# Kernel tuning notes

Measured on AMD Instinct MI355X. Metric: run time of the kernel, lower is better.

## Reference

```python
import jax, jax.numpy as jnp
import numpy as np

B, T, D, U = 32, 2048, 1024, 1024

def setup_inputs() -> dict:
    key = jax.random.key(0)
    ks = jax.random.split(key, 8)
    s = 0.02
    return {
        "query": jax.random.normal(ks[0], (B, D), dtype=jnp.float32),
        "values": jax.random.normal(ks[1], (B, T, D), dtype=jnp.float32),
        "W1": jax.random.normal(ks[2], (D, U), dtype=jnp.float32) * s,
        "b1": jnp.zeros((U,), dtype=jnp.float32),
        "W2": jax.random.normal(ks[3], (D, U), dtype=jnp.float32) * s,
        "b2": jnp.zeros((U,), dtype=jnp.float32),
        "V": jax.random.normal(ks[4], (U, 1), dtype=jnp.float32) * s,
        "bv": jnp.zeros((1,), dtype=jnp.float32),
    }

def reference(query, values, W1, b1, W2, b2, V, bv):
    # query: [B, D] -> [B, 1, U] via W2; values: [B, T, D] -> [B, T, U] via W1
    q_proj = query @ W2 + b2                     # [B, U]
    v_proj = jnp.einsum('btd,du->btu', values, W1) + b1   # [B, T, U]
    # score: Dense(1) on tanh(sum) -> [B, T, 1]
    score = jnp.tanh(v_proj + q_proj[:, None, :]) @ V + bv  # [B, T, 1]
    attention_weights = jax.nn.softmax(score, axis=1)        # softmax over time
    context_vector = jnp.sum(attention_weights * values, axis=1)  # [B, D]
    return context_vector, attention_weights
```

## Files before the change

kernel.cpp:

```cpp
#include <hip/hip_runtime.h>
#include <hip/hip_bf16.h>
#include <stdint.h>

#define WS_W1F   0
#define WS_QP2   2097152
#define WS_SCORE (2097152 + 131072)

typedef __attribute__((ext_vector_type(8))) short bf16x8;
typedef __attribute__((ext_vector_type(4))) float f32x4;

__device__ inline uint16_t f2b(float f) {
    __hip_bfloat16 h = __float2bfloat16(f);
    return *reinterpret_cast<uint16_t*>(&h);
}

__global__ __launch_bounds__(256) void k_prep(const float* __restrict__ W1,
                                              const float* __restrict__ query,
                                              const float* __restrict__ W2,
                                              const float* __restrict__ b1,
                                              const float* __restrict__ b2,
                                              __hip_bfloat16* __restrict__ W1f,
                                              float* __restrict__ qp2,
                                              float* __restrict__ ctx_out) {
    int blk = blockIdx.x, tid = threadIdx.x;
    if (blk < 256) {
        int lane = tid & 63, fi = tid >> 6;
        int l15 = lane & 15, quad = lane >> 4;
        #pragma unroll
        for (int p = 0; p < 2; ++p) {
            int frag = blk * 8 + p * 4 + fi;
            int ut = frag >> 5, ks = frag & 31;
            union { uint16_t h[8]; int4 v; } pk;
            #pragma unroll
            for (int j = 0; j < 8; ++j) {
                float x = W1[(size_t)(ks * 32 + quad * 8 + j) * 1024 + ut * 16 + l15];
                pk.h[j] = f2b(x);
            }
            *(int4*)((char*)W1f + (size_t)frag * 1024 + lane * 16) = pk.v;
        }
    } else {
        int b = blk - 256;
        int u = tid * 4;
        *(float4*)(ctx_out + b * 1024 + u) = make_float4(0.f, 0.f, 0.f, 0.f);
        float4 a;
        a.x = b1[u] + b2[u];     a.y = b1[u+1] + b2[u+1];
        a.z = b1[u+2] + b2[u+2]; a.w = b1[u+3] + b2[u+3];
        const float* q = query + b * 1024;
        #pragma unroll 8
        for (int d = 0; d < 1024; ++d) {
            float qd = q[d];
            float4 wv = *(const float4*)(W2 + (size_t)d * 1024 + u);
            a.x += qd * wv.x; a.y += qd * wv.y; a.z += qd * wv.z; a.w += qd * wv.w;
        }
        *(float4*)(qp2 + b * 1024 + u) = a;
    }
}

__global__ __launch_bounds__(512, 1) void k_score(
        const float* __restrict__ values, const __hip_bfloat16* __restrict__ W1f,
        const float* __restrict__ qp2, const float* __restrict__ V,
        float* __restrict__ score) {
    extern __shared__ char smem[];
    uint16_t* Al = (uint16_t*)smem;
    float* red = (float*)(smem + 131072);

    const int tid = threadIdx.x;
    const int lane = tid & 63, w = tid >> 6;
    const int quad = lane >> 4, l15 = lane & 15;
    const int b = blockIdx.x >> 5, trow0 = (blockIdx.x & 31) << 6;

    const float* Ag = values + (size_t)(b * 2048 + trow0) * 1024;
    #pragma unroll
    for (int i = 0; i < 16; ++i) {
        int id = i * 512 + tid;
        int row = id >> 7, c = id & 127;
        const float* src = Ag + (size_t)row * 1024 + c * 8;
        float4 v0 = *(const float4*)src;
        float4 v1 = *(const float4*)(src + 4);
        union { uint16_t h[8]; int4 v; } pk;
        pk.h[0]=f2b(v0.x); pk.h[1]=f2b(v0.y); pk.h[2]=f2b(v0.z); pk.h[3]=f2b(v0.w);
        pk.h[4]=f2b(v1.x); pk.h[5]=f2b(v1.y); pk.h[6]=f2b(v1.z); pk.h[7]=f2b(v1.w);
        int pos = (c & 112) | ((c & 15) ^ (row & 15));
        *(int4*)(Al + (size_t)row * 1024 + pos * 8) = pk.v;
    }
    __syncthreads();

    const char* Bbase = (const char*)W1f + (size_t)(w * 8) * 32768 + lane * 16;

    f32x4 acc[4][8];
    #pragma unroll
    for (int rt = 0; rt < 4; ++rt)
        #pragma unroll
        for (int ct = 0; ct < 8; ++ct) acc[rt][ct] = (f32x4){0.f, 0.f, 0.f, 0.f};

    bf16x8 af[2][4], bfr[2][8];
    {
        int pos = (quad & 15) ^ l15;
        #pragma unroll
        for (int rt = 0; rt < 4; ++rt)
            af[0][rt] = *(bf16x8*)(Al + (rt * 16 + l15) * 1024 + pos * 8);
        #pragma unroll
        for (int ct = 0; ct < 8; ++ct)
            bfr[0][ct] = *(const bf16x8*)(Bbase + (size_t)(ct * 32) * 1024);
    }

    #pragma unroll 2
    for (int ks = 0; ks < 32; ++ks) {
        int cur = ks & 1, nxt = cur ^ 1;
        if (ks < 31) {
            int cb = (ks + 1) * 4 + quad;
            int pos = (cb & 112) | ((cb & 15) ^ l15);
            #pragma unroll
            for (int rt = 0; rt < 4; ++rt)
                af[nxt][rt] = *(bf16x8*)(Al + (rt * 16 + l15) * 1024 + pos * 8);
            #pragma unroll
            for (int ct = 0; ct < 8; ++ct)
                bfr[nxt][ct] = *(const bf16x8*)(Bbase + (size_t)(ct * 32 + ks + 1) * 1024);
        }
        #pragma unroll
        for (int rt = 0; rt < 4; ++rt)
            #pragma unroll
            for (int ct = 0; ct < 8; ++ct)
                acc[rt][ct] = __builtin_amdgcn_mfma_f32_16x16x32_bf16(
                    af[cur][rt], bfr[cur][ct], acc[rt][ct], 0, 0, 0);
    }

    float srow[4][4];
    #pragma unroll
    for (int rt = 0; rt < 4; ++rt)
        #pragma unroll
        for (int r = 0; r < 4; ++r) srow[rt][r] = 0.f;
    #pragma unroll
    for (int ct = 0; ct < 8; ++ct) {
        int u = w * 128 + ct * 16 + l15;
        float qv = qp2[b * 1024 + u];
        float vv = V[u];
        #pragma unroll
        for (int rt = 0; rt < 4; ++rt)
            #pragma unroll
            for (int r = 0; r < 4; ++r) {
                float x = acc[rt][ct][r] + qv;
                float e = __expf(2.f * x);
                float t = 1.f - 2.f * __builtin_amdgcn_rcpf(1.f + e);
                srow[rt][r] += t * vv;
            }
    }

    #pragma unroll
    for (int rt = 0; rt < 4; ++rt)
        #pragma unroll
        for (int r = 0; r < 4; ++r) {
            float s = srow[rt][r];
            s += __shfl_xor(s, 1, 64);
            s += __shfl_xor(s, 2, 64);
            s += __shfl_xor(s, 4, 64);
            s += __shfl_xor(s, 8, 64);
            srow[rt][r] = s;
        }
    if (l15 == 0) {
        #pragma unroll
        for (int rt = 0; rt < 4; ++rt)
            #pragma unroll
            for (int r = 0; r < 4; ++r)
                red[w * 64 + rt * 16 + quad * 4 + r] = srow[rt][r];
    }
    __syncthreads();
    if (tid < 64) {
        float s = 0.f;
        #pragma unroll
        for (int k = 0; k < 8; ++k) s += red[k * 64 + tid];
        score[b * 2048 + trow0 + tid] = s;
    }
}

__global__ __launch_bounds__(256) void k_out(const float* __restrict__ values,
                                             const float* __restrict__ score,
                                             float* __restrict__ out) {
    __shared__ float red[8];
    __shared__ float wl[128];
    int b = blockIdx.x >> 4, ts = blockIdx.x & 15, tid = threadIdx.x;
    const float* sc = score + b * 2048;
    float s[8]; float m = -1e30f;
    #pragma unroll
    for (int j = 0; j < 8; ++j) {
        s[j] = sc[j * 256 + tid];
        m = fmaxf(m, s[j]);
    }
    for (int off = 32; off; off >>= 1) m = fmaxf(m, __shfl_xor(m, off, 64));
    if ((tid & 63) == 0) red[tid >> 6] = m;
    __syncthreads();
    m = fmaxf(fmaxf(red[0], red[1]), fmaxf(red[2], red[3]));
    float sum = 0.f;
    #pragma unroll
    for (int j = 0; j < 8; ++j) sum += __expf(s[j] - m);
    for (int off = 32; off; off >>= 1) sum += __shfl_xor(sum, off, 64);
    if ((tid & 63) == 0) red[4 + (tid >> 6)] = sum;
    __syncthreads();
    sum = red[4] + red[5] + red[6] + red[7];
    float inv = __builtin_amdgcn_rcpf(sum);
    if (tid < 128) {
        float wv = __expf(sc[ts * 128 + tid] - m) * inv;
        wl[tid] = wv;
        out[32768 + b * 2048 + ts * 128 + tid] = wv;
    }
    __syncthreads();
    const float* vb = values + ((size_t)(b * 2048 + ts * 128)) * 1024 + tid * 4;
    float4 a = {0.f, 0.f, 0.f, 0.f};
    #pragma unroll 4
    for (int t = 0; t < 128; ++t) {
        float4 v = *(const float4*)(vb + (size_t)t * 1024);
        float ww = wl[t];
        a.x += ww * v.x; a.y += ww * v.y; a.z += ww * v.z; a.w += ww * v.w;
    }
    float* o = out + b * 1024 + tid * 4;
    atomicAdd(o + 0, a.x); atomicAdd(o + 1, a.y);
    atomicAdd(o + 2, a.z); atomicAdd(o + 3, a.w);
}

extern "C" void kernel_launch(void* const* d_in, const int* in_sizes, int n_in,
                              void* d_out, int out_size, void* d_ws, size_t ws_size,
                              hipStream_t stream) {
    const float* query  = (const float*)d_in[0];
    const float* values = (const float*)d_in[1];
    const float* W1 = (const float*)d_in[2];
    const float* b1 = (const float*)d_in[3];
    const float* W2 = (const float*)d_in[4];
    const float* b2 = (const float*)d_in[5];
    const float* V  = (const float*)d_in[6];

    char* ws = (char*)d_ws;
    __hip_bfloat16* W1f = (__hip_bfloat16*)(ws + WS_W1F);
    float* qp2   = (float*)(ws + WS_QP2);
    float* score = (float*)(ws + WS_SCORE);
    float* out = (float*)d_out;

    (void)hipFuncSetAttribute((const void*)k_score,
                              hipFuncAttributeMaxDynamicSharedMemorySize, 133120);

    k_prep<<<288, 256, 0, stream>>>(W1, query, W2, b1, b2, W1f, qp2, out);
    k_score<<<1024, 512, 133120, stream>>>(values, W1f, qp2, V, score);
    k_out<<<512, 256, 0, stream>>>(values, score, out);
}
```

Measured before the change: 583.9 us.

## Fuse softmax-weighted context reduction into score kernel with deferred normalization

The score kernel now exponentiates scores directly, with no max subtraction, and immediately accumulates the weighted sum of its values tile. Each block writes a partial context and partial denominator, and a small final kernel sums the partials and normalizes. This removes the second full pass over the large values tensor in the old output kernel. In exchange, softmax loses max-stabilization, relying on the scores staying bounded. The query projection is also split across more blocks, with the query staged in shared memory.

Measured after the change: 579.8 us. No clear change (-0.7%).

```diff
diff --git a/kernel.cpp b/kernel.cpp
--- a/kernel.cpp
+++ b/kernel.cpp
@@ -4,7 +4,10 @@
 
 #define WS_W1F   0
 #define WS_QP2   2097152
-#define WS_SCORE (2097152 + 131072)
+#define WS_ESC   (WS_QP2 + 131072)
+#define WS_PCTX  (WS_ESC + 262144)
+#define WS_PDEN  (WS_PCTX + 4194304)
+#define WS_NEED  (WS_PDEN + 4096)
 
 typedef __attribute__((ext_vector_type(8))) short bf16x8;
 typedef __attribute__((ext_vector_type(4))) float f32x4;
@@ -21,7 +24,9 @@
                                               const float* __restrict__ b2,
                                               __hip_bfloat16* __restrict__ W1f,
                                               float* __restrict__ qp2,
-                                              float* __restrict__ ctx_out) {
+                                              float* __restrict__ zctx,
+                                              float* __restrict__ zden) {
+    __shared__ float qs[1024];
     int blk = blockIdx.x, tid = threadIdx.x;
     if (blk < 256) {
         int lane = tid & 63, fi = tid >> 6;
@@ -39,27 +44,30 @@
             *(int4*)((char*)W1f + (size_t)frag * 1024 + lane * 16) = pk.v;
         }
     } else {
-        int b = blk - 256;
-        int u = tid * 4;
-        *(float4*)(ctx_out + b * 1024 + u) = make_float4(0.f, 0.f, 0.f, 0.f);
-        float4 a;
-        a.x = b1[u] + b2[u];     a.y = b1[u+1] + b2[u+1];
-        a.z = b1[u+2] + b2[u+2]; a.w = b1[u+3] + b2[u+3];
+        int bq = blk - 256;
+        int b = bq >> 2, qc = bq & 3;
+        if (zctx != nullptr && qc == 0) {
+            *(float4*)(zctx + b * 1024 + tid * 4) = make_float4(0.f, 0.f, 0.f, 0.f);
+            if (b == 0 && tid < 32) zden[tid] = 0.f;
+        }
+        int u = qc * 256 + tid;
         const float* q = query + b * 1024;
+        #pragma unroll
+        for (int i = 0; i < 4; ++i) qs[i * 256 + tid] = q[i * 256 + tid];
+        __syncthreads();
+        float a = b1[u] + b2[u];
         #pragma unroll 8
-        for (int d = 0; d < 1024; ++d) {
-            float qd = q[d];
-            float4 wv = *(const float4*)(W2 + (size_t)d * 1024 + u);
-            a.x += qd * wv.x; a.y += qd * wv.y; a.z += qd * wv.z; a.w += qd * wv.w;
-        }
-        *(float4*)(qp2 + b * 1024 + u) = a;
+        for (int d = 0; d < 1024; ++d)
+            a += qs[d] * W2[(size_t)d * 1024 + u];
+        qp2[b * 1024 + u] = a;
     }
 }
 
 __global__ __launch_bounds__(512, 1) void k_score(
         const float* __restrict__ values, const __hip_bfloat16* __restrict__ W1f,
         const float* __restrict__ qp2, const float* __restrict__ V,
-        float* __restrict__ score) {
+        float* __restrict__ escore, float* __restrict__ pctx,
+        float* __restrict__ pden, float* __restrict__ ctxa) {
     extern __shared__ char smem[];
     uint16_t* Al = (uint16_t*)smem;
     float* red = (float*)(smem + 131072);
@@ -165,56 +173,84 @@
                 red[w * 64 + rt * 16 + quad * 4 + r] = srow[rt][r];
     }
     __syncthreads();
+
+    float* wl = (float*)smem;
     if (tid < 64) {
         float s = 0.f;
         #pragma unroll
         for (int k = 0; k < 8; ++k) s += red[k * 64 + tid];
-        score[b * 2048 + trow0 + tid] = s;
-    }
-}
-
-__global__ __launch_bounds__(256) void k_out(const float* __restrict__ values,
-                                             const float* __restrict__ score,
-                                             float* __restrict__ out) {
-    __shared__ float red[8];
-    __shared__ float wl[128];
-    int b = blockIdx.x >> 4, ts = blockIdx.x & 15, tid = threadIdx.x;
-    const float* sc = score + b * 2048;
-    float s[8]; float m = -1e30f;
-    #pragma unroll
-    for (int j = 0; j < 8; ++j) {
-        s[j] = sc[j * 256 + tid];
-        m = fmaxf(m, s[j]);
-    }
-    for (int off = 32; off; off >>= 1) m = fmaxf(m, __shfl_xor(m, off, 64));
-    if ((tid & 63) == 0) red[tid >> 6] = m;
-    __syncthreads();
-    m = fmaxf(fmaxf(red[0], red[1]), fmaxf(red[2], red[3]));
-    float sum = 0.f;
-    #pragma unroll
-    for (int j = 0; j < 8; ++j) sum += __expf(s[j] - m);
-    for (int off = 32; off; off >>= 1) sum += __shfl_xor(sum, off, 64);
-    if ((tid & 63) == 0) red[4 + (tid >> 6)] = sum;
-    __syncthreads();
-    sum = red[4] + red[5] + red[6] + red[7];
-    float inv = __builtin_amdgcn_rcpf(sum);
-    if (tid < 128) {
-        float wv = __expf(sc[ts * 128 + tid] - m) * inv;
-        wl[tid] = wv;
-        out[32768 + b * 2048 + ts * 128 + tid] = wv;
-    }
-    __syncthreads();
-    const float* vb = values + ((size_t)(b * 2048 + ts * 128)) * 1024 + tid * 4;
-    float4 a = {0.f, 0.f, 0.f, 0.f};
-    #pragma unroll 4
-    for (int t = 0; t < 128; ++t) {
-        float4 v = *(const float4*)(vb + (size_t)t * 1024);
-        float ww = wl[t];
-        a.x += ww * v.x; a.y += ww * v.y; a.z += ww * v.z; a.w += ww * v.w;
-    }
-    float* o = out + b * 1024 + tid * 4;
-    atomicAdd(o + 0, a.x); atomicAdd(o + 1, a.y);
-    atomicAdd(o + 2, a.z); atomicAdd(o + 3, a.w);
+        float e = __expf(s);
+        escore[b * 2048 + trow0 + tid] = e;
+        wl[tid] = e;
+        float dsum = e;
+        #pragma unroll
+        for (int off = 32; off; off >>= 1) dsum += __shfl_xor(dsum, off, 64);
+        if (tid == 0) {
+            if (pctx != nullptr) pden[blockIdx.x] = dsum;
+            else                 atomicAdd(&pden[b], dsum);
+        }
+    }
+    __syncthreads();
+
+    {
+        const float* Vg = values + (size_t)(b * 2048 + trow0) * 1024 + tid * 2;
+        float ax = 0.f, ay = 0.f;
+        #pragma unroll 8
+        for (int t = 0; t < 64; ++t) {
+            float wv = wl[t];
+            float2 v = *(const float2*)(Vg + (size_t)t * 1024);
+            ax += wv * v.x; ay += wv * v.y;
+        }
+        if (pctx != nullptr) {
+            *(float2*)(pctx + (size_t)blockIdx.x * 1024 + tid * 2) = make_float2(ax, ay);
+        } else {
+            float* o = ctxa + b * 1024 + tid * 2;
+            atomicAdd(o + 0, ax);
+            atomicAdd(o + 1, ay);
+        }
+    }
+}
+
+__global__ __launch_bounds__(256) void k_final(const float* __restrict__ pctx,
+                                               const float* __restrict__ pden,
+                                               const float* __restrict__ escore,
+                                               float* __restrict__ out) {
+    __shared__ float sinv;
+    int b = blockIdx.x, tid = threadIdx.x;
+    if (tid == 0) {
+        float dsum = 0.f;
+        if (pctx != nullptr) {
+            #pragma unroll
+            for (int t = 0; t < 32; ++t) dsum += pden[b * 32 + t];
+        } else {
+            dsum = pden[b];
+        }
+        sinv = 1.f / dsum;
+    }
+    __syncthreads();
+    float inv = sinv;
+
+    int d = tid * 4;
+    if (pctx != nullptr) {
+        float4 a = {0.f, 0.f, 0.f, 0.f};
+        #pragma unroll 8
+        for (int t = 0; t < 32; ++t) {
+            float4 p = *(const float4*)(pctx + (size_t)(b * 32 + t) * 1024 + d);
+            a.x += p.x; a.y += p.y; a.z += p.z; a.w += p.w;
+        }
+        a.x *= inv; a.y *= inv; a.z *= inv; a.w *= inv;
+        *(float4*)(out + b * 1024 + d) = a;
+    } else {
+        float4 a = *(const float4*)(out + b * 1024 + d);
+        a.x *= inv; a.y *= inv; a.z *= inv; a.w *= inv;
+        *(float4*)(out + b * 1024 + d) = a;
+    }
+
+    #pragma unroll
+    for (int i = 0; i < 8; ++i) {
+        int t = i * 256 + tid;
+        out[32768 + b * 2048 + t] = escore[b * 2048 + t] * inv;
+    }
 }
 
 extern "C" void kernel_launch(void* const* d_in, const int* in_sizes, int n_in,
@@ -230,14 +266,20 @@
 
     char* ws = (char*)d_ws;
     __hip_bfloat16* W1f = (__hip_bfloat16*)(ws + WS_W1F);
-    float* qp2   = (float*)(ws + WS_QP2);
-    float* score = (float*)(ws + WS_SCORE);
+    float* qp2 = (float*)(ws + WS_QP2);
     float* out = (float*)d_out;
+
+    const bool big = ws_size >= (size_t)WS_NEED;
+    float* escore = big ? (float*)(ws + WS_ESC)  : out + 32768;
+    float* pctx   = big ? (float*)(ws + WS_PCTX) : nullptr;
+    float* pden   = big ? (float*)(ws + WS_PDEN) : (float*)(ws + WS_ESC);
+    float* zctx   = big ? nullptr : out;
+    float* zden   = big ? nullptr : pden;
 
     (void)hipFuncSetAttribute((const void*)k_score,
                               hipFuncAttributeMaxDynamicSharedMemorySize, 133120);
 
-    k_prep<<<288, 256, 0, stream>>>(W1, query, W2, b1, b2, W1f, qp2, out);
-    k_score<<<1024, 512, 133120, stream>>>(values, W1f, qp2, V, score);
-    k_out<<<512, 256, 0, stream>>>(values, score, out);
-}
+    k_prep<<<384, 256, 0, stream>>>(W1, query, W2, b1, b2, W1f, qp2, zctx, zden);
+    k_score<<<1024, 512, 133120, stream>>>(values, W1f, qp2, V, escore, pctx, pden, out);
+    k_final<<<32, 256, 0, stream>>>(pctx, pden, escore, out);
+}
```
